# Kernel optimization log

Hardware: AMD Instinct MI355X
Metric: run time of the kernel (lower is better)

The kernel has to match this reference:

```python
import jax, jax.numpy as jnp
import numpy as np

B, S, EMBED, HEADS, FFN = 8, 2048, 1024, 256, 4096
EPS = 1e-5


def circuit_expvals(params):
    # Closed form of the 4-qubit PennyLane circuit.
    # RZ(x_i) on |0> is a global phase -> output is independent of the data input x.
    # After the RY layer, <Z_i> = cos(params_i) = c_i. Conjugating Z_i through the
    # CNOT ring [0,1],[1,2],[2,3],[3,0] (Heisenberg picture) gives:
    #   Z0 -> Z1 Z2 Z3, Z1 -> Z0 Z1, Z2 -> Z0 Z1 Z2, Z3 -> Z0 Z1 Z2 Z3
    c = jnp.cos(params)
    return jnp.stack([
        c[1] * c[2] * c[3],
        c[0] * c[1],
        c[0] * c[1] * c[2],
        c[0] * c[1] * c[2] * c[3],
    ])


def layer_norm(x, g, b):
    m = jnp.mean(x, axis=-1, keepdims=True)
    v = jnp.mean((x - m) ** 2, axis=-1, keepdims=True)
    return g * (x - m) * jax.lax.rsqrt(v + EPS) + b


def setup_inputs() -> dict:
    key = jax.random.key(0)
    k = jax.random.split(key, 10)
    sc = EMBED ** -0.5
    return {
        "x": jax.random.normal(k[0], (B, S, EMBED), jnp.float32),
        "wq": jax.random.normal(k[1], (EMBED, EMBED), jnp.float32) * sc,
        "wk": jax.random.normal(k[2], (EMBED, EMBED), jnp.float32) * sc,
        "wv": jax.random.normal(k[3], (EMBED, EMBED), jnp.float32) * sc,
        "w_mix": jax.random.normal(k[4], (EMBED, EMBED), jnp.float32) * sc,
        "attn_params": jax.random.normal(k[5], (4,), jnp.float32),
        "w1": jax.random.normal(k[6], (4, EMBED), jnp.float32) * sc,
        "w2": jax.random.normal(k[7], (FFN, 4), jnp.float32) * 0.5,
        "w_out": jax.random.normal(k[8], (EMBED, FFN), jnp.float32) * (FFN ** -0.5),
        "ffn_params": jax.random.normal(k[9], (4,), jnp.float32),
        "ln1_g": jnp.ones((EMBED,), jnp.float32),
        "ln1_b": jnp.zeros((EMBED,), jnp.float32),
        "ln2_g": jnp.ones((EMBED,), jnp.float32),
        "ln2_b": jnp.zeros((EMBED,), jnp.float32),
    }


def reference(x, wq, wk, wv, w_mix, attn_params, w1, w2, w_out, ffn_params,
              ln1_g, ln1_b, ln2_g, ln2_b):
    # Dropout layers are identity in eval mode.
    # --- QuantumAttention ---
    # The circuit expvals ignore their data input (RZ on |0> is a global phase),
    # so q_q = k_q = v_q = cvec broadcast over (batch, heads, seq, 4). Scores are
    # therefore constant, softmax is uniform over seq, and attn @ v_q == cvec.
    # (wq/wk/wv projections have no effect on the output; grads w.r.t. them are 0.)
    cvec = circuit_expvals(attn_params)                 # (4,)
    heads_out = jnp.tile(cvec, HEADS)                   # (EMBED,) = concat over heads
    attn_out = heads_out @ w_mix.T                      # (EMBED,), constant per token
    x1 = layer_norm(x + attn_out, ln1_g, ln1_b)         # (B, S, EMBED)
    # --- QuantumFeedForward ---
    # linear1 output feeds only the RZ layer -> no effect; circuit output is constant.
    cvec_f = circuit_expvals(ffn_params)                # (4,)
    ffn_out = jax.nn.relu(cvec_f @ w2.T) @ w_out.T      # (EMBED,), constant per token
    return layer_norm(x1 + ffn_out, ln2_g, ln2_b)
```

## Files before the change

### kernel.cpp

```cpp
#include <hip/hip_runtime.h>
#include <math.h>

#define EMBED 1024
#define FFN_DIM 4096
#define TOKENS (8 * 2048)
#define EPS 1e-5f

typedef __attribute__((ext_vector_type(4))) float f32x4;

__device__ __forceinline__ void circuit_cvec(const float* p, float cv[4]) {
    float c0 = cosf(p[0]);
    float c1 = cosf(p[1]);
    float c2 = cosf(p[2]);
    float c3 = cosf(p[3]);
    cv[0] = c1 * c2 * c3;
    cv[1] = c0 * c1;
    cv[2] = c0 * c1 * c2;
    cv[3] = c0 * c1 * c2 * c3;
}

__global__ __launch_bounds__(256) void k_hidden(const float* __restrict__ w2,
                                                const float* __restrict__ ffn_p,
                                                float* __restrict__ h) {
    int f = blockIdx.x * 256 + threadIdx.x;
    float cv[4];
    circuit_cvec(ffn_p, cv);
    f32x4 row = *(const f32x4*)(w2 + f * 4);
    float s = row.x * cv[0] + row.y * cv[1] + row.z * cv[2] + row.w * cv[3];
    h[f] = s > 0.f ? s : 0.f;
}

__global__ __launch_bounds__(256) void k_const(const float* __restrict__ w_mix,
                                               const float* __restrict__ attn_p,
                                               const float* __restrict__ w_out,
                                               const float* __restrict__ h,
                                               float* __restrict__ attn_out,
                                               float* __restrict__ ffn_out) {
    int e = blockIdx.x * 4 + (threadIdx.x >> 6);
    int lane = threadIdx.x & 63;
    float cv[4];
    circuit_cvec(attn_p, cv);

    float sa = 0.f;
    const float* wm = w_mix + e * EMBED + lane * 16;
    #pragma unroll
    for (int c = 0; c < 4; ++c) {
        f32x4 u = *(const f32x4*)(wm + c * 4);
        sa += u.x * cv[0] + u.y * cv[1] + u.z * cv[2] + u.w * cv[3];
    }

    float sf = 0.f;
    const float* wo = w_out + e * FFN_DIM + lane * 64;
    const float* hp = h + lane * 64;
    #pragma unroll
    for (int c = 0; c < 16; ++c) {
        f32x4 u = *(const f32x4*)(wo + c * 4);
        f32x4 hv = *(const f32x4*)(hp + c * 4);
        sf += u.x * hv.x + u.y * hv.y + u.z * hv.z + u.w * hv.w;
    }

    #pragma unroll
    for (int m = 32; m >= 1; m >>= 1) {
        sa += __shfl_xor(sa, m, 64);
        sf += __shfl_xor(sf, m, 64);
    }
    if (lane == 0) {
        attn_out[e] = sa;
        ffn_out[e] = sf;
    }
}

__global__ __launch_bounds__(256) void k_main(const float* __restrict__ x,
                                              const float* __restrict__ attn_out,
                                              const float* __restrict__ ffn_out,
                                              const float* __restrict__ g1,
                                              const float* __restrict__ b1,
                                              const float* __restrict__ g2,
                                              const float* __restrict__ b2,
                                              float* __restrict__ out) {
    int token = blockIdx.x * 4 + (threadIdx.x >> 6);
    int lane = threadIdx.x & 63;
    const int base = token * EMBED;

    float y[16];
    float s = 0.f, s2 = 0.f;
    #pragma unroll
    for (int c = 0; c < 4; ++c) {
        int off = c * 256 + lane * 4;
        f32x4 u = *(const f32x4*)(x + base + off);
        f32x4 a = *(const f32x4*)(attn_out + off);
        #pragma unroll
        for (int k = 0; k < 4; ++k) {
            float v = u[k] + a[k];
            y[c * 4 + k] = v;
            s += v;
            s2 += v * v;
        }
    }
    #pragma unroll
    for (int m = 32; m >= 1; m >>= 1) {
        s += __shfl_xor(s, m, 64);
        s2 += __shfl_xor(s2, m, 64);
    }
    float m1 = s * (1.f / EMBED);
    float rs1 = rsqrtf(s2 * (1.f / EMBED) - m1 * m1 + EPS);

    float z[16];
    float t = 0.f, t2 = 0.f;
    #pragma unroll
    for (int c = 0; c < 4; ++c) {
        int off = c * 256 + lane * 4;
        f32x4 ug = *(const f32x4*)(g1 + off);
        f32x4 ub = *(const f32x4*)(b1 + off);
        f32x4 fo = *(const f32x4*)(ffn_out + off);
        #pragma unroll
        for (int k = 0; k < 4; ++k) {
            float x1 = ug[k] * (y[c * 4 + k] - m1) * rs1 + ub[k];
            float v = x1 + fo[k];
            z[c * 4 + k] = v;
            t += v;
            t2 += v * v;
        }
    }
    #pragma unroll
    for (int m = 32; m >= 1; m >>= 1) {
        t += __shfl_xor(t, m, 64);
        t2 += __shfl_xor(t2, m, 64);
    }
    float m2 = t * (1.f / EMBED);
    float rs2 = rsqrtf(t2 * (1.f / EMBED) - m2 * m2 + EPS);

    #pragma unroll
    for (int c = 0; c < 4; ++c) {
        int off = c * 256 + lane * 4;
        f32x4 ug = *(const f32x4*)(g2 + off);
        f32x4 ub = *(const f32x4*)(b2 + off);
        f32x4 o;
        #pragma unroll
        for (int k = 0; k < 4; ++k) {
            o[k] = ug[k] * (z[c * 4 + k] - m2) * rs2 + ub[k];
        }
        *(f32x4*)(out + base + off) = o;
    }
}

extern "C" void kernel_launch(void* const* d_in, const int* in_sizes, int n_in,
                              void* d_out, int out_size, void* d_ws, size_t ws_size,
                              hipStream_t stream) {
    const float* x      = (const float*)d_in[0];
    const float* w_mix  = (const float*)d_in[4];
    const float* attn_p = (const float*)d_in[5];
    const float* w2     = (const float*)d_in[7];
    const float* w_out  = (const float*)d_in[8];
    const float* ffn_p  = (const float*)d_in[9];
    const float* ln1_g  = (const float*)d_in[10];
    const float* ln1_b  = (const float*)d_in[11];
    const float* ln2_g  = (const float*)d_in[12];
    const float* ln2_b  = (const float*)d_in[13];
    float* out = (float*)d_out;

    float* ws_f     = (float*)d_ws;
    float* attn_out = ws_f;
    float* ffn_out  = ws_f + 1024;
    float* h        = ws_f + 2048;

    k_hidden<<<FFN_DIM / 256, 256, 0, stream>>>(w2, ffn_p, h);
    k_const<<<EMBED / 4, 256, 0, stream>>>(w_mix, attn_p, w_out, h, attn_out, ffn_out);
    k_main<<<TOKENS / 4, 256, 0, stream>>>(x, attn_out, ffn_out,
                                           ln1_g, ln1_b, ln2_g, ln2_b, out);
}
```

Before: 172.9 us.

## Fold second LayerNorm statistics algebraically into a single reduction pass

Each block of the constant kernel now recomputes the hidden FFN vector in shared memory, which removes the separate hidden kernel. It also precomputes per-feature products and global scalar sums through atomics. The main kernel gets the second LayerNorm mean and variance in closed form from extra dot-product accumulators, so one cross-lane reduction replaces two dependent ones. It also writes the output with nontemporal stores. In exchange, each token needs more accumulators and loads, and the closed-form variance may lose precision through cancellation.

Result: slower. 235.9 us (+36.4%).

```diff
diff --git a/kernel.cpp b/kernel.cpp
--- a/kernel.cpp
+++ b/kernel.cpp
@@ -19,44 +19,56 @@
     cv[3] = c0 * c1 * c2 * c3;
 }
 
-__global__ __launch_bounds__(256) void k_hidden(const float* __restrict__ w2,
-                                                const float* __restrict__ ffn_p,
-                                                float* __restrict__ h) {
-    int f = blockIdx.x * 256 + threadIdx.x;
-    float cv[4];
-    circuit_cvec(ffn_p, cv);
-    f32x4 row = *(const f32x4*)(w2 + f * 4);
-    float s = row.x * cv[0] + row.y * cv[1] + row.z * cv[2] + row.w * cv[3];
-    h[f] = s > 0.f ? s : 0.f;
+
+__global__ __launch_bounds__(64) void k_zero(float* __restrict__ scal) {
+    if (threadIdx.x < 8) scal[threadIdx.x] = 0.f;
 }
 
 __global__ __launch_bounds__(256) void k_const(const float* __restrict__ w_mix,
                                                const float* __restrict__ attn_p,
+                                               const float* __restrict__ w2,
                                                const float* __restrict__ w_out,
-                                               const float* __restrict__ h,
-                                               float* __restrict__ attn_out,
-                                               float* __restrict__ ffn_out) {
-    int e = blockIdx.x * 4 + (threadIdx.x >> 6);
-    int lane = threadIdx.x & 63;
-    float cv[4];
-    circuit_cvec(attn_p, cv);
+                                               const float* __restrict__ ffn_p,
+                                               const float* __restrict__ g1v,
+                                               const float* __restrict__ b1v,
+                                               const float* __restrict__ g2v,
+                                               const float* __restrict__ b2v,
+                                               float* __restrict__ ws) {
+    __shared__ float h[FFN_DIM];
+    int tid = threadIdx.x;
+    float cvf[4], cva[4];
+    circuit_cvec(ffn_p, cvf);
+    circuit_cvec(attn_p, cva);
+
+    #pragma unroll
+    for (int i = 0; i < 16; ++i) {
+        int f = i * 256 + tid;
+        f32x4 r = *(const f32x4*)(w2 + f * 4);
+        float s = r.x * cvf[0] + r.y * cvf[1] + r.z * cvf[2] + r.w * cvf[3];
+        h[f] = s > 0.f ? s : 0.f;
+    }
+    __syncthreads();
+
+    int e = blockIdx.x * 4 + (tid >> 6);
+    int lane = tid & 63;
 
     float sa = 0.f;
-    const float* wm = w_mix + e * EMBED + lane * 16;
+    const float* wm = w_mix + e * EMBED;
     #pragma unroll
     for (int c = 0; c < 4; ++c) {
-        f32x4 u = *(const f32x4*)(wm + c * 4);
-        sa += u.x * cv[0] + u.y * cv[1] + u.z * cv[2] + u.w * cv[3];
+        int idx = c * 256 + lane * 4;
+        f32x4 v = *(const f32x4*)(wm + idx);
+        sa += v.x * cva[0] + v.y * cva[1] + v.z * cva[2] + v.w * cva[3];
     }
 
     float sf = 0.f;
-    const float* wo = w_out + e * FFN_DIM + lane * 64;
-    const float* hp = h + lane * 64;
+    const float* wo = w_out + e * FFN_DIM;
     #pragma unroll
     for (int c = 0; c < 16; ++c) {
-        f32x4 u = *(const f32x4*)(wo + c * 4);
-        f32x4 hv = *(const f32x4*)(hp + c * 4);
-        sf += u.x * hv.x + u.y * hv.y + u.z * hv.z + u.w * hv.w;
+        int idx = c * 256 + lane * 4;
+        f32x4 v = *(const f32x4*)(wo + idx);
+        f32x4 hv = *(const f32x4*)(h + idx);
+        sf += v.x * hv.x + v.y * hv.y + v.z * hv.z + v.w * hv.w;
     }
 
     #pragma unroll
@@ -64,83 +76,98 @@
         sa += __shfl_xor(sa, m, 64);
         sf += __shfl_xor(sf, m, 64);
     }
+
     if (lane == 0) {
-        attn_out[e] = sa;
-        ffn_out[e] = sf;
+        float g1 = g1v[e], b1 = b1v[e], g2 = g2v[e], b2 = b2v[e];
+        float u = b1 + sf;
+        ws[e] = sa;
+        ws[1024 + e] = u;
+        ws[2048 + e] = g1 * g2;
+        ws[3072 + e] = g2 * u;
+        float* scal = ws + 4096;
+        atomicAdd(scal + 0, g1);
+        atomicAdd(scal + 1, u);
+        atomicAdd(scal + 2, g1 * g1);
+        atomicAdd(scal + 3, g1 * u);
+        atomicAdd(scal + 4, u * u);
     }
 }
 
 __global__ __launch_bounds__(256) void k_main(const float* __restrict__ x,
-                                              const float* __restrict__ attn_out,
-                                              const float* __restrict__ ffn_out,
-                                              const float* __restrict__ g1,
-                                              const float* __restrict__ b1,
-                                              const float* __restrict__ g2,
-                                              const float* __restrict__ b2,
+                                              const float* __restrict__ g1v,
+                                              const float* __restrict__ g2v,
+                                              const float* __restrict__ b2v,
+                                              const float* __restrict__ ws,
                                               float* __restrict__ out) {
     int token = blockIdx.x * 4 + (threadIdx.x >> 6);
     int lane = threadIdx.x & 63;
     const int base = token * EMBED;
 
+    const float* attn = ws;
+    const float* uvec = ws + 1024;
+    const float* E1v = ws + 2048;
+    const float* E2v = ws + 3072;
+    const float* scal = ws + 4096;
+    float Sg1 = scal[0], Su = scal[1], Sg12 = scal[2], Sg1u = scal[3], Su2 = scal[4];
+
     float y[16];
-    float s = 0.f, s2 = 0.f;
+    float s = 0.f, s2 = 0.f, p = 0.f, p2 = 0.f, q = 0.f, pu = 0.f;
     #pragma unroll
     for (int c = 0; c < 4; ++c) {
         int off = c * 256 + lane * 4;
-        f32x4 u = *(const f32x4*)(x + base + off);
-        f32x4 a = *(const f32x4*)(attn_out + off);
+        f32x4 xv = *(const f32x4*)(x + base + off);
+        f32x4 av = *(const f32x4*)(attn + off);
+        f32x4 gv = *(const f32x4*)(g1v + off);
+        f32x4 uv = *(const f32x4*)(uvec + off);
         #pragma unroll
         for (int k = 0; k < 4; ++k) {
-            float v = u[k] + a[k];
-            y[c * 4 + k] = v;
-            s += v;
-            s2 += v * v;
+            float yy = xv[k] + av[k];
+            float w = gv[k] * yy;
+            y[c * 4 + k] = yy;
+            s += yy;
+            s2 = fmaf(yy, yy, s2);
+            p += w;
+            p2 = fmaf(w, w, p2);
+            q = fmaf(gv[k], w, q);
+            pu = fmaf(w, uv[k], pu);
         }
     }
+
     #pragma unroll
     for (int m = 32; m >= 1; m >>= 1) {
         s += __shfl_xor(s, m, 64);
         s2 += __shfl_xor(s2, m, 64);
+        p += __shfl_xor(p, m, 64);
+        p2 += __shfl_xor(p2, m, 64);
+        q += __shfl_xor(q, m, 64);
+        pu += __shfl_xor(pu, m, 64);
     }
-    float m1 = s * (1.f / EMBED);
-    float rs1 = rsqrtf(s2 * (1.f / EMBED) - m1 * m1 + EPS);
 
-    float z[16];
-    float t = 0.f, t2 = 0.f;
+    const float rN = 1.f / EMBED;
+    float m1 = s * rN;
+    float rs1 = rsqrtf(s2 * rN - m1 * m1 + EPS);
+    float t = rs1 * (p - m1 * Sg1) + Su;
+    float t2 = rs1 * rs1 * (p2 - 2.f * m1 * q + m1 * m1 * Sg12)
+             + 2.f * rs1 * (pu - m1 * Sg1u) + Su2;
+    float m2 = t * rN;
+    float rs2 = rsqrtf(t2 * rN - m2 * m2 + EPS);
+
+    float A = rs1 * rs2;
+    float B = m2 * rs2;
     #pragma unroll
     for (int c = 0; c < 4; ++c) {
         int off = c * 256 + lane * 4;
-        f32x4 ug = *(const f32x4*)(g1 + off);
-        f32x4 ub = *(const f32x4*)(b1 + off);
-        f32x4 fo = *(const f32x4*)(ffn_out + off);
-        #pragma unroll
-        for (int k = 0; k < 4; ++k) {
-            float x1 = ug[k] * (y[c * 4 + k] - m1) * rs1 + ub[k];
-            float v = x1 + fo[k];
-            z[c * 4 + k] = v;
-            t += v;
-            t2 += v * v;
-        }
-    }
-    #pragma unroll
-    for (int m = 32; m >= 1; m >>= 1) {
-        t += __shfl_xor(t, m, 64);
-        t2 += __shfl_xor(t2, m, 64);
-    }
-    float m2 = t * (1.f / EMBED);
-    float rs2 = rsqrtf(t2 * (1.f / EMBED) - m2 * m2 + EPS);
-
-    #pragma unroll
-    for (int c = 0; c < 4; ++c) {
-        int off = c * 256 + lane * 4;
-        f32x4 ug = *(const f32x4*)(g2 + off);
-        f32x4 ub = *(const f32x4*)(b2 + off);
+        f32x4 e1 = *(const f32x4*)(E1v + off);
+        f32x4 e2 = *(const f32x4*)(E2v + off);
+        f32x4 g2 = *(const f32x4*)(g2v + off);
+        f32x4 b2 = *(const f32x4*)(b2v + off);
         f32x4 o;
         #pragma unroll
         for (int k = 0; k < 4; ++k) {
-            o[k] = ug[k] * (z[c * 4 + k] - m2) * rs2 + ub[k];
+            float base2 = fmaf(rs2, e2[k], fmaf(-B, g2[k], b2[k]));
+            o[k] = fmaf(A * e1[k], y[c * 4 + k] - m1, base2);
         }
-        *(f32x4*)(out + base + off) = o;
+        __builtin_nontemporal_store(o, (f32x4*)(out + base + off));
     }
 }
 
@@ -158,14 +185,10 @@
     const float* ln2_g  = (const float*)d_in[12];
     const float* ln2_b  = (const float*)d_in[13];
     float* out = (float*)d_out;
+    float* ws  = (float*)d_ws;
 
-    float* ws_f     = (float*)d_ws;
-    float* attn_out = ws_f;
-    float* ffn_out  = ws_f + 1024;
-    float* h        = ws_f + 2048;
-
-    k_hidden<<<FFN_DIM / 256, 256, 0, stream>>>(w2, ffn_p, h);
-    k_const<<<EMBED / 4, 256, 0, stream>>>(w_mix, attn_p, w_out, h, attn_out, ffn_out);
-    k_main<<<TOKENS / 4, 256, 0, stream>>>(x, attn_out, ffn_out,
-                                           ln1_g, ln1_b, ln2_g, ln2_b, out);
+    k_zero<<<1, 64, 0, stream>>>(ws + 4096);
+    k_const<<<EMBED / 4, 256, 0, stream>>>(w_mix, attn_p, w2, w_out, ffn_p,
+                                           ln1_g, ln1_b, ln2_g, ln2_b, ws);
+    k_main<<<TOKENS / 4, 256, 0, stream>>>(x, ln1_g, ln2_g, ln2_b, ws, out);
 }
```
